# Performance work log

Hardware: AMD Instinct MI355X
Metric: run time of the kernel (lower is better)

## Reference

```python
import jax, jax.numpy as jnp
import numpy as np

T_MEDIA = 3      # torch.arange(3)
N_LATENTS = 64   # repeat(..., m=64)
H = 8            # rearrange h=8
D_HEAD = 64


def setup_inputs() -> dict:
    key = jax.random.key(0)
    ks = jax.random.split(key, 6)
    B, S = 4, 2048
    Dv, Dt = 2048, 4096
    inner = H * D_HEAD  # 512
    latent = jax.random.normal(ks[0], (B, T_MEDIA, N_LATENTS, Dv), dtype=jnp.float32)
    y = jax.random.normal(ks[1], (B, S, Dt), dtype=jnp.float32)
    media_mask = jax.random.randint(ks[2], (B, S), 0, T_MEDIA + 1)  # values in {0,1,2,3}
    W_vk = jax.random.normal(ks[3], (Dv, 2 * inner), dtype=jnp.float32) / np.sqrt(Dv)
    W_q = jax.random.normal(ks[4], (Dt, inner), dtype=jnp.float32) / np.sqrt(Dt)
    W_out = jax.random.normal(ks[5], (inner, Dt), dtype=jnp.float32) / np.sqrt(inner)
    return {"latent": latent, "y": y, "media_mask": media_mask,
            "W_vk": W_vk, "W_q": W_q, "W_out": W_out}


def reference(latent, y, media_mask, W_vk, W_q, W_out):
    B, T, N, Dv = latent.shape
    S = y.shape[1]
    # b t n d -> b (t n) d
    vf = latent.reshape(B, T * N, Dv)
    kv = vf @ W_vk                      # [B, TN, 2*H*Dh]
    k, v = jnp.split(kv, 2, axis=-1)
    q = y @ W_q                         # [B, S, H*Dh]
    def to_heads(x):
        b, n, _ = x.shape
        return x.reshape(b, n, H, D_HEAD).transpose(0, 2, 1, 3)  # b h n d
    q, k, v = to_heads(q), to_heads(k), to_heads(v)
    # NOTE: original applies no 1/sqrt(d) scaling (self.temp unused)
    sim = jnp.einsum('bhid,bhjd->bhij', q, k)   # [B, H, S, T*N]
    media_time = jnp.arange(T) + 1                               # [T]
    key_time = jnp.repeat(media_time, N)                         # [T*N]
    t2m = media_mask[:, None, :, None] == key_time[None, None, None, :]
    neg = -jnp.finfo(sim.dtype).max
    sim = jnp.where(t2m, sim, neg)
    logits = jax.nn.softmax(sim, axis=-1)
    no_media = (media_mask == 0)[:, None, :, None]
    logits = jnp.where(no_media, 0.0, logits)
    out = jnp.einsum('bhij,bhjd->bhid', logits, v)               # [B, H, S, Dh]
    out = out.transpose(0, 2, 1, 3).reshape(B, S, H * D_HEAD)
    return out @ W_out
```

## Files before the change

kernel.cpp:

```cpp
#include <hip/hip_runtime.h>
#include <hip/hip_bf16.h>

typedef __attribute__((ext_vector_type(4))) float f32x4;
typedef __attribute__((ext_vector_type(8))) short bf16x8;
typedef __attribute__((ext_vector_type(4))) unsigned short u16x4;
typedef __attribute__((ext_vector_type(8))) unsigned short u16x8;

#define QCAP 8256
#define QSTR ((size_t)QCAP * 512)
#define KVB 384

__device__ __forceinline__ unsigned short f2bf(float f) {
  unsigned int u = __builtin_bit_cast(unsigned int, f);
  unsigned int r = (u + 0x7FFFu + ((u >> 16) & 1u)) >> 16;
  return (unsigned short)r;
}
__device__ __forceinline__ float bf2f(unsigned short h) {
  unsigned int u = ((unsigned int)h) << 16;
  return __builtin_bit_cast(float, u);
}

__device__ __forceinline__ void gload_lds16(const void* g, void* l) {
  __builtin_amdgcn_global_load_lds(
      (__attribute__((address_space(1))) unsigned int*)g,
      (__attribute__((address_space(3))) unsigned int*)l, 16, 0, 0);
}

__global__ __launch_bounds__(256) void gather_rows(const int* __restrict__ mask,
                                                   int* __restrict__ cnt,
                                                   int* __restrict__ idx,
                                                   int* __restrict__ mcnt,
                                                   int* __restrict__ mlist) {
  int g = blockIdx.x * 256 + threadIdx.x;
  int m = mask[g];
  if (m > 0) {
    int bt = (g >> 11) * 3 + m - 1;
    int p = atomicAdd(&cnt[bt], 1);
    idx[bt * 2048 + p] = g;
  } else {
    int p = atomicAdd(mcnt, 1);
    mlist[p] = g;
  }
}

__global__ __launch_bounds__(256) void scan_build(const int* __restrict__ cnt,
                                                  int* __restrict__ offs,
                                                  const int* __restrict__ idx,
                                                  int* __restrict__ glob) {
  __shared__ int so[13];
  if (threadIdx.x == 0) {
    int s = 0;
#pragma unroll
    for (int i = 0; i < 12; ++i) {
      so[i] = s;
      s += cnt[i];
    }
    so[12] = s;
    if (blockIdx.x == 0)
#pragma unroll
      for (int i = 0; i < 13; ++i) offs[i] = so[i];
  }
  __syncthreads();
  int bt = blockIdx.x;
  int n = cnt[bt], o = so[bt];
  for (int j = threadIdx.x; j < n; j += 256) glob[o + j] = idx[bt * 2048 + j];
}

__global__ __launch_bounds__(256) void prep_all(
    const float* __restrict__ y, const int* __restrict__ glob,
    const int* __restrict__ offs, unsigned short* __restrict__ ybf,
    const float* __restrict__ Wq, const float* __restrict__ Wvk,
    const float* __restrict__ Wo, const float* __restrict__ latent,
    unsigned short* __restrict__ QTh, unsigned short* __restrict__ VKh,
    unsigned short* __restrict__ VKl, unsigned short* __restrict__ OTh,
    unsigned short* __restrict__ latbf) {
  int bid = blockIdx.x;
  if (bid < 16384) {
    int p = bid >> 1, half = bid & 1;
    if (p >= offs[12]) return;
    int g = glob[p];
    const float* src = y + (size_t)g * 4096 + half * 2048 + threadIdx.x * 8;
    unsigned short* dst = ybf + (size_t)p * 4096 + half * 2048 + threadIdx.x * 8;
    f32x4 a = *(const f32x4*)src;
    f32x4 b = *(const f32x4*)(src + 4);
    u16x8 o;
#pragma unroll
    for (int j = 0; j < 4; ++j) o[j] = f2bf(a[j]);
#pragma unroll
    for (int j = 0; j < 4; ++j) o[4 + j] = f2bf(b[j]);
    *(u16x8*)dst = o;
    return;
  }
  if (bid >= 22528) {
    long i = ((long)(bid - 22528) * 256 + threadIdx.x) * 8;
    f32x4 a = *(const f32x4*)(latent + i);
    f32x4 b = *(const f32x4*)(latent + i + 4);
    u16x8 o;
#pragma unroll
    for (int j = 0; j < 4; ++j) o[j] = f2bf(a[j]);
#pragma unroll
    for (int j = 0; j < 4; ++j) o[4 + j] = f2bf(b[j]);
    *(u16x8*)(latbf + i) = o;
    return;
  }
  int wb = bid - 16384;
  __shared__ float tile[32][33];
  const float* W;
  unsigned short *Th, *Tl;
  int K, N, nbx, b;
  if (wb < 2048) {
    W = Wq; Th = QTh; Tl = nullptr; K = 4096; N = 512; nbx = 16; b = wb;
  } else if (wb < 4096) {
    W = Wvk; Th = VKh; Tl = VKl; K = 2048; N = 1024; nbx = 32; b = wb - 2048;
  } else {
    W = Wo; Th = OTh; Tl = nullptr; K = 512; N = 4096; nbx = 128; b = wb - 4096;
  }
  int n0 = (b % nbx) * 32, k0 = (b / nbx) * 32;
  int tx = threadIdx.x & 31, ty = threadIdx.x >> 5;
#pragma unroll
  for (int r = 0; r < 4; ++r)
    tile[ty + 8 * r][tx] = W[(size_t)(k0 + ty + 8 * r) * N + n0 + tx];
  __syncthreads();
#pragma unroll
  for (int r = 0; r < 4; ++r) {
    float f = tile[tx][ty + 8 * r];
    unsigned short hi = f2bf(f);
    size_t o = (size_t)(n0 + ty + 8 * r) * K + k0 + tx;
    Th[o] = hi;
    if (Tl) Tl[o] = f2bf(f - bf2f(hi));
  }
}

__global__ __launch_bounds__(256) void kv_finish(const float* __restrict__ kvp,
                                                 unsigned short* __restrict__ Kh,
                                                 unsigned short* __restrict__ Kl,
                                                 unsigned short* __restrict__ Vt) {
  int row = blockIdx.x;
  int bt = row >> 6, key = row & 63;
  int c = threadIdx.x * 4;
  const float* p = kvp + (size_t)row * 1024 + c;
  f32x4 v = *(const f32x4*)p;
#pragma unroll
  for (int sl = 1; sl < 8; ++sl)
    v += *(const f32x4*)(p + (size_t)sl * 768 * 1024);
  if (c < 512) {
    int h = c >> 6, d = c & 63;
    u16x4 hv, lv;
#pragma unroll
    for (int j = 0; j < 4; ++j) {
      unsigned short hi = f2bf(v[j]);
      hv[j] = hi;
      lv[j] = f2bf(v[j] - bf2f(hi));
    }
    size_t o = ((size_t)(bt * 8 + h) * 64 + key) * 64 + d;
    *(u16x4*)&Kh[o] = hv;
    *(u16x4*)&Kl[o] = lv;
  } else {
    int cc = c - 512;
    int h = cc >> 6, d = cc & 63;
#pragma unroll
    for (int j = 0; j < 4; ++j)
      Vt[((size_t)(bt * 8 + h) * 64 + d + j) * 64 + key] = f2bf(v[j]);
  }
}

#define BM 128
#define BN 128
#define BK 64

__global__ __launch_bounds__(256) void gemm_dual(
    const unsigned short* __restrict__ latbf, const unsigned short* __restrict__ VKh,
    const unsigned short* __restrict__ VKl, const unsigned short* __restrict__ ybf,
    const unsigned short* __restrict__ QTh, float* __restrict__ kvp,
    float* __restrict__ qc, const int* __restrict__ offs) {
  __shared__ unsigned short smem[BM * BK + BN * BK + 64];
  unsigned short* Ald = smem;
  unsigned short* Bhld = smem + BM * BK;
  float* epi = (float*)smem;

  int tid = threadIdx.x, lane = tid & 63, wid = tid >> 6;
  int wr = wid >> 1, wc = wid & 1;
  const unsigned short *Ab, *Bb;
  float* Cv;
  int N, K, kbeg, kend, bm, bn;
  size_t outOff;
  if (blockIdx.x < KVB) {
    int w = (blockIdx.x & 7) * (KVB >> 3) + (blockIdx.x >> 3);
    bm = w / 64;
    int r = w % 64;
    bn = r >> 3;
    int slice = r & 7, ks = slice & 3;
    Ab = latbf + (size_t)(bm * BM) * 2048;
    Bb = (slice < 4 ? VKh : VKl) + (size_t)(bn * BN) * 2048;
    Cv = kvp;
    N = 1024;
    K = 2048;
    kbeg = ks * 512;
    kend = kbeg + 512;
    outOff = (size_t)slice * 768 * 1024;
  } else {
    int qb = blockIdx.x - KVB;
    int w = (qb & 7) * 64 + (qb >> 3);
    bm = w & 63;
    int r = w >> 6;
    bn = r >> 1;
    int ks = r & 1;
    if (bm * BM >= offs[12]) return;
    Ab = ybf + (size_t)(bm * BM) * 4096;
    Bb = QTh + (size_t)(bn * BN) * 4096;
    Cv = qc;
    N = 512;
    K = 4096;
    kbeg = ks * 2048;
    kend = kbeg + 2048;
    outOff = (size_t)ks * QSTR;
  }

  int fr = lane & 15, fq = lane >> 4;
  int srow = lane >> 3, scol = ((lane & 7) ^ (lane >> 3)) * 8;

  f32x4 acc[4][4];
#pragma unroll
  for (int i = 0; i < 4; ++i)
#pragma unroll
    for (int j = 0; j < 4; ++j) acc[i][j] = (f32x4){0.f, 0.f, 0.f, 0.f};

  for (int k0 = kbeg; k0 < kend; k0 += BK) {
#pragma unroll
    for (int i = 0; i < 4; ++i) {
      int c = wid * 4 + i;
      size_t go = (size_t)(c * 8 + srow) * K + k0 + scol;
      gload_lds16(Ab + go, &Ald[c * 512]);
      gload_lds16(Bb + go, &Bhld[c * 512]);
    }
    __syncthreads();
#pragma unroll
    for (int kk = 0; kk < 2; ++kk) {
      int ca = (kk * 32 + fq * 8) ^ ((fr & 7) * 8);
      bf16x8 af[4], bf[4];
#pragma unroll
      for (int i = 0; i < 4; ++i) {
        af[i] = *(const bf16x8*)&Ald[(wr * 64 + i * 16 + fr) * BK + ca];
        bf[i] = *(const bf16x8*)&Bhld[(wc * 64 + i * 16 + fr) * BK + ca];
      }
#pragma unroll
      for (int mi = 0; mi < 4; ++mi)
#pragma unroll
        for (int ni = 0; ni < 4; ++ni)
          acc[mi][ni] = __builtin_amdgcn_mfma_f32_16x16x32_bf16(
              af[mi], bf[ni], acc[mi][ni], 0, 0, 0);
    }
    __syncthreads();
  }

#pragma unroll 1
  for (int p = 0; p < 2; ++p) {
    __syncthreads();
    if (wr == p) {
#pragma unroll
      for (int mi = 0; mi < 4; ++mi)
#pragma unroll
        for (int ni = 0; ni < 4; ++ni)
#pragma unroll
          for (int r = 0; r < 4; ++r) {
            int lrow = mi * 16 + fq * 4 + r;
            int lcol = wc * 64 + ni * 16 + fr;
            int pc = lcol ^ ((lrow & 7) << 4);
            epi[lrow * 128 + pc] = acc[mi][ni][r];
          }
    }
    __syncthreads();
#pragma unroll
    for (int k = 0; k < 8; ++k) {
      int chunk = k * 256 + tid;
      int lrow = chunk >> 5;
      int c4 = (chunk & 31) * 4;
      int pc4 = c4 ^ ((lrow & 7) << 4);
      f32x4 v = *(f32x4*)&epi[lrow * 128 + pc4];
      int row = bm * BM + p * 64 + lrow;
      *(f32x4*)&Cv[outOff + (size_t)row * N + bn * BN + c4] = v;
    }
  }
}

__global__ __launch_bounds__(256) void gemm_out(
    const unsigned short* __restrict__ A, const unsigned short* __restrict__ Bh,
    float* __restrict__ Cv, const int* __restrict__ glob,
    const int* __restrict__ offs, const int* __restrict__ mcnt,
    const int* __restrict__ mlist, int M, int N, int K) {
  __shared__ unsigned short smem[BM * BK + BN * BK + 64];
  unsigned short* Ald = smem;
  unsigned short* Bhld = smem + BM * BK;
  float* epi = (float*)smem;

  int tid = threadIdx.x, lane = tid & 63, wid = tid >> 6;
  int wr = wid >> 1, wc = wid & 1;
  int nwg = gridDim.x;
  int w = (blockIdx.x & 7) * (nwg >> 3) + (blockIdx.x >> 3);
  int nTN = N / BN;
  int nBM = M / BM;
  int bm = w % nBM;
  int bn = w / nBM;
  int mv = offs[12];

  if (bm * BM >= mv) {
    int bmLive = (mv + BM - 1) / BM;
    int nDead = (nBM - bmLive) * nTN;
    int deadIdx = (bm - bmLive) + bn * (nBM - bmLive);
    int nm = *mcnt;
    f32x4 z = (f32x4){0.f, 0.f, 0.f, 0.f};
    for (int j = deadIdx; j < nm; j += nDead) {
      float* row = Cv + (size_t)mlist[j] * N;
#pragma unroll
      for (int i = 0; i < 4; ++i) *(f32x4*)&row[(i * 256 + tid) * 4] = z;
    }
    return;
  }

  const unsigned short* Ab = A + (size_t)(bm * BM) * K;
  const unsigned short* Bhb = Bh + (size_t)(bn * BN) * K;
  int fr = lane & 15, fq = lane >> 4;
  int srow = lane >> 3, scol = ((lane & 7) ^ (lane >> 3)) * 8;

  f32x4 acc[4][4];
#pragma unroll
  for (int i = 0; i < 4; ++i)
#pragma unroll
    for (int j = 0; j < 4; ++j) acc[i][j] = (f32x4){0.f, 0.f, 0.f, 0.f};

  for (int k0 = 0; k0 < K; k0 += BK) {
#pragma unroll
    for (int i = 0; i < 4; ++i) {
      int c = wid * 4 + i;
      size_t go = (size_t)(c * 8 + srow) * K + k0 + scol;
      gload_lds16(Ab + go, &Ald[c * 512]);
      gload_lds16(Bhb + go, &Bhld[c * 512]);
    }
    __syncthreads();
#pragma unroll
    for (int kk = 0; kk < 2; ++kk) {
      int ca = (kk * 32 + fq * 8) ^ ((fr & 7) * 8);
      bf16x8 af[4], bf[4];
#pragma unroll
      for (int i = 0; i < 4; ++i) {
        af[i] = *(const bf16x8*)&Ald[(wr * 64 + i * 16 + fr) * BK + ca];
        bf[i] = *(const bf16x8*)&Bhld[(wc * 64 + i * 16 + fr) * BK + ca];
      }
#pragma unroll
      for (int mi = 0; mi < 4; ++mi)
#pragma unroll
        for (int ni = 0; ni < 4; ++ni)
          acc[mi][ni] = __builtin_amdgcn_mfma_f32_16x16x32_bf16(
              af[mi], bf[ni], acc[mi][ni], 0, 0, 0);
    }
    __syncthreads();
  }

#pragma unroll 1
  for (int p = 0; p < 2; ++p) {
    __syncthreads();
    if (wr == p) {
#pragma unroll
      for (int mi = 0; mi < 4; ++mi)
#pragma unroll
        for (int ni = 0; ni < 4; ++ni)
#pragma unroll
          for (int r = 0; r < 4; ++r) {
            int lrow = mi * 16 + fq * 4 + r;
            int lcol = wc * 64 + ni * 16 + fr;
            int pc = lcol ^ ((lrow & 7) << 4);
            epi[lrow * 128 + pc] = acc[mi][ni][r];
          }
    }
    __syncthreads();
#pragma unroll
    for (int k = 0; k < 8; ++k) {
      int chunk = k * 256 + tid;
      int lrow = chunk >> 5;
      int c4 = (chunk & 31) * 4;
      int pc4 = c4 ^ ((lrow & 7) << 4);
      f32x4 v = *(f32x4*)&epi[lrow * 128 + pc4];
      int row = bm * BM + p * 64 + lrow;
      if (row < mv)
        *(f32x4*)&Cv[(size_t)glob[row] * N + bn * BN + c4] = v;
    }
  }

  int bmLive = (mv + BM - 1) / BM;
  if (bmLive == nBM && bm == 0) {
    int nm = *mcnt;
    f32x4 z = (f32x4){0.f, 0.f, 0.f, 0.f};
    for (int j = bn; j < nm; j += nTN) {
      float* row = Cv + (size_t)mlist[j] * N;
#pragma unroll
      for (int i = 0; i < 4; ++i) *(f32x4*)&row[(i * 256 + tid) * 4] = z;
    }
  }
}

__global__ __launch_bounds__(256) void attn5(
    const float* __restrict__ qc, const unsigned short* __restrict__ Kh,
    const unsigned short* __restrict__ Kl, const unsigned short* __restrict__ Vt,
    const int* __restrict__ cnt, const int* __restrict__ offs,
    unsigned short* __restrict__ attnc) {
  __shared__ unsigned short Pl[4][32][72];
  int tid = threadIdx.x, wid = tid >> 6, lane = tid & 63;
  int fr = lane & 15, fq = lane >> 4;
  int bt = blockIdx.x >> 6, rt = blockIdx.x & 63;
  int n = cnt[bt];
  int rbase = rt * 32;
  if (rbase >= n) return;
  int qbase = offs[bt] + rbase;

#pragma unroll 1
  for (int hp = 0; hp < 2; ++hp) {
    int h = wid * 2 + hp;
    const unsigned short* khb = Kh + ((size_t)(bt * 8 + h) * 64) * 64;
    const unsigned short* klb = Kl + ((size_t)(bt * 8 + h) * 64) * 64;
    const unsigned short* vtb = Vt + ((size_t)(bt * 8 + h) * 64) * 64;

    f32x4 sacc[2][4];
#pragma unroll
    for (int i = 0; i < 2; ++i)
#pragma unroll
      for (int j = 0; j < 4; ++j) sacc[i][j] = (f32x4){0.f, 0.f, 0.f, 0.f};

#pragma unroll
    for (int kk = 0; kk < 2; ++kk) {
      bf16x8 qh[2], ql[2];
#pragma unroll
      for (int mi = 0; mi < 2; ++mi) {
        size_t qo = (size_t)(qbase + mi * 16 + fr) * 512 + h * 64 + kk * 32 + fq * 8;
        f32x4 s0 = *(const f32x4*)(qc + qo) + *(const f32x4*)(qc + QSTR + qo);
        f32x4 s1 = *(const f32x4*)(qc + qo + 4) +
                   *(const f32x4*)(qc + QSTR + qo + 4);
        float sv[8];
        *(f32x4*)&sv[0] = s0;
        *(f32x4*)&sv[4] = s1;
#pragma unroll
        for (int j = 0; j < 8; ++j) {
          unsigned short hi = f2bf(sv[j]);
          qh[mi][j] = (short)hi;
          ql[mi][j] = (short)f2bf(sv[j] - bf2f(hi));
        }
      }
#pragma unroll
      for (int ni = 0; ni < 4; ++ni) {
        size_t ko = (size_t)(ni * 16 + fr) * 64 + kk * 32 + fq * 8;
        bf16x8 kh = *(const bf16x8*)(khb + ko);
        bf16x8 kl = *(const bf16x8*)(klb + ko);
#pragma unroll
        for (int mi = 0; mi < 2; ++mi) {
          sacc[mi][ni] = __builtin_amdgcn_mfma_f32_16x16x32_bf16(
              qh[mi], kh, sacc[mi][ni], 0, 0, 0);
          sacc[mi][ni] = __builtin_amdgcn_mfma_f32_16x16x32_bf16(
              qh[mi], kl, sacc[mi][ni], 0, 0, 0);
          sacc[mi][ni] = __builtin_amdgcn_mfma_f32_16x16x32_bf16(
              ql[mi], kh, sacc[mi][ni], 0, 0, 0);
        }
      }
    }

#pragma unroll
    for (int mi = 0; mi < 2; ++mi) {
#pragma unroll
      for (int r = 0; r < 4; ++r) {
        float m = fmaxf(fmaxf(sacc[mi][0][r], sacc[mi][1][r]),
                        fmaxf(sacc[mi][2][r], sacc[mi][3][r]));
#pragma unroll
        for (int o = 1; o < 16; o <<= 1) m = fmaxf(m, __shfl_xor(m, o));
        float e0 = __expf(sacc[mi][0][r] - m);
        float e1 = __expf(sacc[mi][1][r] - m);
        float e2 = __expf(sacc[mi][2][r] - m);
        float e3 = __expf(sacc[mi][3][r] - m);
        float s = e0 + e1 + e2 + e3;
#pragma unroll
        for (int o = 1; o < 16; o <<= 1) s += __shfl_xor(s, o);
        float inv = 1.f / s;
        int row = mi * 16 + fq * 4 + r;
        Pl[wid][row][fr] = f2bf(e0 * inv);
        Pl[wid][row][16 + fr] = f2bf(e1 * inv);
        Pl[wid][row][32 + fr] = f2bf(e2 * inv);
        Pl[wid][row][48 + fr] = f2bf(e3 * inv);
      }
    }

    f32x4 oacc[2][4];
#pragma unroll
    for (int i = 0; i < 2; ++i)
#pragma unroll
      for (int j = 0; j < 4; ++j) oacc[i][j] = (f32x4){0.f, 0.f, 0.f, 0.f};
#pragma unroll
    for (int kk = 0; kk < 2; ++kk) {
      bf16x8 pa[2];
#pragma unroll
      for (int mi = 0; mi < 2; ++mi)
        pa[mi] = *(const bf16x8*)&Pl[wid][mi * 16 + fr][kk * 32 + fq * 8];
#pragma unroll
      for (int ni = 0; ni < 4; ++ni) {
        bf16x8 vb = *(const bf16x8*)(vtb + (size_t)(ni * 16 + fr) * 64 +
                                     kk * 32 + fq * 8);
#pragma unroll
        for (int mi = 0; mi < 2; ++mi)
          oacc[mi][ni] = __builtin_amdgcn_mfma_f32_16x16x32_bf16(
              pa[mi], vb, oacc[mi][ni], 0, 0, 0);
      }
    }

#pragma unroll
    for (int mi = 0; mi < 2; ++mi)
#pragma unroll
      for (int r = 0; r < 4; ++r) {
        int row = mi * 16 + fq * 4 + r;
        if (rbase + row < n) {
          unsigned short* ar = attnc + (size_t)(qbase + row) * 512 + h * 64 + fr;
          ar[0] = f2bf(oacc[mi][0][r]);
          ar[16] = f2bf(oacc[mi][1][r]);
          ar[32] = f2bf(oacc[mi][2][r]);
          ar[48] = f2bf(oacc[mi][3][r]);
        }
      }
  }
}

extern "C" void kernel_launch(void* const* d_in, const int* in_sizes, int n_in,
                              void* d_out, int out_size, void* d_ws,
                              size_t ws_size, hipStream_t stream) {
  const float* latent = (const float*)d_in[0];
  const float* y = (const float*)d_in[1];
  const int* mask = (const int*)d_in[2];
  const float* W_vk = (const float*)d_in[3];
  const float* W_q = (const float*)d_in[4];
  const float* W_out = (const float*)d_in[5];
  float* out = (float*)d_out;

  char* ws = (char*)d_ws;
  size_t off = 0;
  auto alloc = [&](size_t bytes) -> void* {
    void* p = ws + off;
    off = (off + bytes + 255) & ~(size_t)255;
    return p;
  };
  unsigned short* WqT_h = (unsigned short*)alloc((size_t)512 * 4096 * 2);
  unsigned short* WvkT_h = (unsigned short*)alloc((size_t)1024 * 2048 * 2);
  unsigned short* WvkT_l = (unsigned short*)alloc((size_t)1024 * 2048 * 2);
  unsigned short* WoT_h = (unsigned short*)alloc((size_t)4096 * 512 * 2);
  unsigned short* ybf = (unsigned short*)alloc((size_t)8192 * 4096 * 2);
  unsigned short* latbf = (unsigned short*)alloc((size_t)768 * 2048 * 2);
  float* qc = (float*)alloc((size_t)2 * QCAP * 512 * 4);
  float* kvp = (float*)alloc((size_t)8 * 768 * 1024 * 4);
  unsigned short* Khb = (unsigned short*)alloc((size_t)768 * 512 * 2);
  unsigned short* Klb = (unsigned short*)alloc((size_t)768 * 512 * 2);
  unsigned short* Vtb = (unsigned short*)alloc((size_t)768 * 512 * 2);
  unsigned short* attnc = (unsigned short*)alloc((size_t)8192 * 512 * 2);
  int* cntm = (int*)alloc(13 * 4);
  int* cnt = cntm;
  int* mcnt = cntm + 12;
  int* idx = (int*)alloc((size_t)12 * 2048 * 4);
  int* offs = (int*)alloc(13 * 4);
  int* glob = (int*)alloc(8192 * 4);
  int* mlist = (int*)alloc(8192 * 4);

  hipMemsetAsync(cntm, 0, 13 * 4, stream);

  gather_rows<<<32, 256, 0, stream>>>(mask, cnt, idx, mcnt, mlist);
  scan_build<<<12, 256, 0, stream>>>(cnt, offs, idx, glob);

  prep_all<<<23296, 256, 0, stream>>>(y, glob, offs, ybf, W_q, W_vk, W_out,
                                      latent, WqT_h, WvkT_h, WvkT_l, WoT_h,
                                      latbf);

  gemm_dual<<<KVB + 512, 256, 0, stream>>>(latbf, WvkT_h, WvkT_l, ybf, WqT_h,
                                           kvp, qc, offs);
  kv_finish<<<768, 256, 0, stream>>>(kvp, Khb, Klb, Vtb);
  attn5<<<12 * 64, 256, 0, stream>>>(qc, Khb, Klb, Vtb, cnt, offs, attnc);
  gemm_out<<<(8192 / BM) * (4096 / BN), 256, 0, stream>>>(
      attnc, WoT_h, out, glob, offs, mcnt, mlist, 8192, 4096, 512);
}
```

Baseline: 264.8 us.

## Fuse KV split-K reduction into GEMM epilogue and merge gather/scan kernels

The KV projection no longer splits K into 8 slices written to a float partial buffer and reduced by a separate kv_finish kernel. Each of 48 blocks now accumulates the full K over both hi and lo weight passes and writes the bf16 K hi/lo and transposed V directly from registers. The gather and scan kernels plus the memset are replaced by one single-block kernel that uses shared-memory counters. This drops two launches and the partial-sum traffic, but KV parallelism falls from 384 to 48 blocks with a longer serial K loop, and the epilogue uses scattered 2-byte stores.

Result: faster. 211.8 us (median of 2 runs) (-20.0%).

```diff
diff --git a/kernel.cpp b/kernel.cpp
--- a/kernel.cpp
+++ b/kernel.cpp
@@ -3,12 +3,11 @@
 
 typedef __attribute__((ext_vector_type(4))) float f32x4;
 typedef __attribute__((ext_vector_type(8))) short bf16x8;
-typedef __attribute__((ext_vector_type(4))) unsigned short u16x4;
 typedef __attribute__((ext_vector_type(8))) unsigned short u16x8;
 
 #define QCAP 8256
 #define QSTR ((size_t)QCAP * 512)
-#define KVB 384
+#define KVB 48
 
 __device__ __forceinline__ unsigned short f2bf(float f) {
   unsigned int u = __builtin_bit_cast(unsigned int, f);
@@ -26,44 +25,49 @@
       (__attribute__((address_space(3))) unsigned int*)l, 16, 0, 0);
 }
 
-__global__ __launch_bounds__(256) void gather_rows(const int* __restrict__ mask,
-                                                   int* __restrict__ cnt,
-                                                   int* __restrict__ idx,
-                                                   int* __restrict__ mcnt,
-                                                   int* __restrict__ mlist) {
-  int g = blockIdx.x * 256 + threadIdx.x;
-  int m = mask[g];
-  if (m > 0) {
-    int bt = (g >> 11) * 3 + m - 1;
-    int p = atomicAdd(&cnt[bt], 1);
-    idx[bt * 2048 + p] = g;
-  } else {
-    int p = atomicAdd(mcnt, 1);
-    mlist[p] = g;
-  }
-}
-
-__global__ __launch_bounds__(256) void scan_build(const int* __restrict__ cnt,
-                                                  int* __restrict__ offs,
-                                                  const int* __restrict__ idx,
-                                                  int* __restrict__ glob) {
+__global__ __launch_bounds__(1024) void gather_scan(
+    const int* __restrict__ mask, int* __restrict__ offs,
+    int* __restrict__ glob, int* __restrict__ mcnt, int* __restrict__ mlist) {
+  __shared__ int scnt[13];
   __shared__ int so[13];
-  if (threadIdx.x == 0) {
+  int tid = threadIdx.x;
+  if (tid < 13) scnt[tid] = 0;
+  __syncthreads();
+#pragma unroll
+  for (int i = 0; i < 8; ++i) {
+    int g = i * 1024 + tid;
+    int m = mask[g];
+    atomicAdd(&scnt[m > 0 ? (g >> 11) * 3 + m - 1 : 12], 1);
+  }
+  __syncthreads();
+  if (tid == 0) {
     int s = 0;
 #pragma unroll
     for (int i = 0; i < 12; ++i) {
       so[i] = s;
-      s += cnt[i];
+      s += scnt[i];
     }
     so[12] = s;
-    if (blockIdx.x == 0)
-#pragma unroll
-      for (int i = 0; i < 13; ++i) offs[i] = so[i];
+#pragma unroll
+    for (int i = 0; i < 13; ++i) offs[i] = so[i];
+    *mcnt = scnt[12];
   }
   __syncthreads();
-  int bt = blockIdx.x;
-  int n = cnt[bt], o = so[bt];
-  for (int j = threadIdx.x; j < n; j += 256) glob[o + j] = idx[bt * 2048 + j];
+  if (tid < 13) scnt[tid] = 0;
+  __syncthreads();
+#pragma unroll
+  for (int i = 0; i < 8; ++i) {
+    int g = i * 1024 + tid;
+    int m = mask[g];
+    if (m > 0) {
+      int bt = (g >> 11) * 3 + m - 1;
+      int p = atomicAdd(&scnt[bt], 1);
+      glob[so[bt] + p] = g;
+    } else {
+      int p = atomicAdd(&scnt[12], 1);
+      mlist[p] = g;
+    }
+  }
 }
 
 __global__ __launch_bounds__(256) void prep_all(
@@ -131,39 +135,6 @@
   }
 }
 
-__global__ __launch_bounds__(256) void kv_finish(const float* __restrict__ kvp,
-                                                 unsigned short* __restrict__ Kh,
-                                                 unsigned short* __restrict__ Kl,
-                                                 unsigned short* __restrict__ Vt) {
-  int row = blockIdx.x;
-  int bt = row >> 6, key = row & 63;
-  int c = threadIdx.x * 4;
-  const float* p = kvp + (size_t)row * 1024 + c;
-  f32x4 v = *(const f32x4*)p;
-#pragma unroll
-  for (int sl = 1; sl < 8; ++sl)
-    v += *(const f32x4*)(p + (size_t)sl * 768 * 1024);
-  if (c < 512) {
-    int h = c >> 6, d = c & 63;
-    u16x4 hv, lv;
-#pragma unroll
-    for (int j = 0; j < 4; ++j) {
-      unsigned short hi = f2bf(v[j]);
-      hv[j] = hi;
-      lv[j] = f2bf(v[j] - bf2f(hi));
-    }
-    size_t o = ((size_t)(bt * 8 + h) * 64 + key) * 64 + d;
-    *(u16x4*)&Kh[o] = hv;
-    *(u16x4*)&Kl[o] = lv;
-  } else {
-    int cc = c - 512;
-    int h = cc >> 6, d = cc & 63;
-#pragma unroll
-    for (int j = 0; j < 4; ++j)
-      Vt[((size_t)(bt * 8 + h) * 64 + d + j) * 64 + key] = f2bf(v[j]);
-  }
-}
-
 #define BM 128
 #define BN 128
 #define BK 64
@@ -171,7 +142,8 @@
 __global__ __launch_bounds__(256) void gemm_dual(
     const unsigned short* __restrict__ latbf, const unsigned short* __restrict__ VKh,
     const unsigned short* __restrict__ VKl, const unsigned short* __restrict__ ybf,
-    const unsigned short* __restrict__ QTh, float* __restrict__ kvp,
+    const unsigned short* __restrict__ QTh, unsigned short* __restrict__ Kh,
+    unsigned short* __restrict__ Kl, unsigned short* __restrict__ Vt,
     float* __restrict__ qc, const int* __restrict__ offs) {
   __shared__ unsigned short smem[BM * BK + BN * BK + 64];
   unsigned short* Ald = smem;
@@ -180,40 +152,31 @@
 
   int tid = threadIdx.x, lane = tid & 63, wid = tid >> 6;
   int wr = wid >> 1, wc = wid & 1;
-  const unsigned short *Ab, *Bb;
-  float* Cv;
-  int N, K, kbeg, kend, bm, bn;
-  size_t outOff;
-  if (blockIdx.x < KVB) {
-    int w = (blockIdx.x & 7) * (KVB >> 3) + (blockIdx.x >> 3);
-    bm = w / 64;
-    int r = w % 64;
-    bn = r >> 3;
-    int slice = r & 7, ks = slice & 3;
+  bool isKV = blockIdx.x < KVB;
+  const unsigned short* Ab;
+  const unsigned short* Bb = nullptr;
+  int K, kbeg, kend, bm, bn, ks = 0;
+  if (isKV) {
+    int sw = (blockIdx.x & 7) * (KVB >> 3) + (blockIdx.x >> 3);
+    bm = sw / 8;
+    bn = sw % 8;
     Ab = latbf + (size_t)(bm * BM) * 2048;
-    Bb = (slice < 4 ? VKh : VKl) + (size_t)(bn * BN) * 2048;
-    Cv = kvp;
-    N = 1024;
     K = 2048;
-    kbeg = ks * 512;
-    kend = kbeg + 512;
-    outOff = (size_t)slice * 768 * 1024;
+    kbeg = 0;
+    kend = 2048;
   } else {
     int qb = blockIdx.x - KVB;
     int w = (qb & 7) * 64 + (qb >> 3);
     bm = w & 63;
     int r = w >> 6;
     bn = r >> 1;
-    int ks = r & 1;
+    ks = r & 1;
     if (bm * BM >= offs[12]) return;
     Ab = ybf + (size_t)(bm * BM) * 4096;
     Bb = QTh + (size_t)(bn * BN) * 4096;
-    Cv = qc;
-    N = 512;
     K = 4096;
     kbeg = ks * 2048;
     kend = kbeg + 2048;
-    outOff = (size_t)ks * QSTR;
   }
 
   int fr = lane & 15, fq = lane >> 4;
@@ -225,32 +188,64 @@
 #pragma unroll
     for (int j = 0; j < 4; ++j) acc[i][j] = (f32x4){0.f, 0.f, 0.f, 0.f};
 
-  for (int k0 = kbeg; k0 < kend; k0 += BK) {
-#pragma unroll
-    for (int i = 0; i < 4; ++i) {
-      int c = wid * 4 + i;
-      size_t go = (size_t)(c * 8 + srow) * K + k0 + scol;
-      gload_lds16(Ab + go, &Ald[c * 512]);
-      gload_lds16(Bb + go, &Bhld[c * 512]);
-    }
-    __syncthreads();
-#pragma unroll
-    for (int kk = 0; kk < 2; ++kk) {
-      int ca = (kk * 32 + fq * 8) ^ ((fr & 7) * 8);
-      bf16x8 af[4], bf[4];
+  int npass = isKV ? 2 : 1;
+#pragma unroll 1
+  for (int pass = 0; pass < npass; ++pass) {
+    const unsigned short* Bp =
+        isKV ? ((pass ? VKl : VKh) + (size_t)(bn * BN) * 2048) : Bb;
+    for (int k0 = kbeg; k0 < kend; k0 += BK) {
 #pragma unroll
       for (int i = 0; i < 4; ++i) {
-        af[i] = *(const bf16x8*)&Ald[(wr * 64 + i * 16 + fr) * BK + ca];
-        bf[i] = *(const bf16x8*)&Bhld[(wc * 64 + i * 16 + fr) * BK + ca];
-      }
-#pragma unroll
-      for (int mi = 0; mi < 4; ++mi)
-#pragma unroll
-        for (int ni = 0; ni < 4; ++ni)
-          acc[mi][ni] = __builtin_amdgcn_mfma_f32_16x16x32_bf16(
-              af[mi], bf[ni], acc[mi][ni], 0, 0, 0);
-    }
-    __syncthreads();
+        int c = wid * 4 + i;
+        size_t go = (size_t)(c * 8 + srow) * K + k0 + scol;
+        gload_lds16(Ab + go, &Ald[c * 512]);
+        gload_lds16(Bp + go, &Bhld[c * 512]);
+      }
+      __syncthreads();
+#pragma unroll
+      for (int kk = 0; kk < 2; ++kk) {
+        int ca = (kk * 32 + fq * 8) ^ ((fr & 7) * 8);
+        bf16x8 af[4], bf[4];
+#pragma unroll
+        for (int i = 0; i < 4; ++i) {
+          af[i] = *(const bf16x8*)&Ald[(wr * 64 + i * 16 + fr) * BK + ca];
+          bf[i] = *(const bf16x8*)&Bhld[(wc * 64 + i * 16 + fr) * BK + ca];
+        }
+#pragma unroll
+        for (int mi = 0; mi < 4; ++mi)
+#pragma unroll
+          for (int ni = 0; ni < 4; ++ni)
+            acc[mi][ni] = __builtin_amdgcn_mfma_f32_16x16x32_bf16(
+                af[mi], bf[ni], acc[mi][ni], 0, 0, 0);
+      }
+      __syncthreads();
+    }
+  }
+
+  if (isKV) {
+#pragma unroll
+    for (int mi = 0; mi < 4; ++mi)
+#pragma unroll
+      for (int ni = 0; ni < 4; ++ni)
+#pragma unroll
+        for (int r = 0; r < 4; ++r) {
+          int row = bm * BM + wr * 64 + mi * 16 + fq * 4 + r;
+          int col = bn * BN + wc * 64 + ni * 16 + fr;
+          int bt = row >> 6, key = row & 63;
+          float v = acc[mi][ni][r];
+          if (col < 512) {
+            int h = col >> 6, d = col & 63;
+            unsigned short hi = f2bf(v);
+            size_t o = ((size_t)(bt * 8 + h) * 64 + key) * 64 + d;
+            Kh[o] = hi;
+            Kl[o] = f2bf(v - bf2f(hi));
+          } else {
+            int c = col - 512;
+            int h = c >> 6, d = c & 63;
+            Vt[((size_t)(bt * 8 + h) * 64 + d) * 64 + key] = f2bf(v);
+          }
+        }
+    return;
   }
 
 #pragma unroll 1
@@ -278,7 +273,7 @@
       int pc4 = c4 ^ ((lrow & 7) << 4);
       f32x4 v = *(f32x4*)&epi[lrow * 128 + pc4];
       int row = bm * BM + p * 64 + lrow;
-      *(f32x4*)&Cv[outOff + (size_t)row * N + bn * BN + c4] = v;
+      *(f32x4*)&qc[(size_t)ks * QSTR + (size_t)row * 512 + bn * BN + c4] = v;
     }
   }
 }
@@ -401,13 +396,12 @@
 __global__ __launch_bounds__(256) void attn5(
     const float* __restrict__ qc, const unsigned short* __restrict__ Kh,
     const unsigned short* __restrict__ Kl, const unsigned short* __restrict__ Vt,
-    const int* __restrict__ cnt, const int* __restrict__ offs,
-    unsigned short* __restrict__ attnc) {
+    const int* __restrict__ offs, unsigned short* __restrict__ attnc) {
   __shared__ unsigned short Pl[4][32][72];
   int tid = threadIdx.x, wid = tid >> 6, lane = tid & 63;
   int fr = lane & 15, fq = lane >> 4;
   int bt = blockIdx.x >> 6, rt = blockIdx.x & 63;
-  int n = cnt[bt];
+  int n = offs[bt + 1] - offs[bt];
   int rbase = rt * 32;
   if (rbase >= n) return;
   int qbase = offs[bt] + rbase;
@@ -548,32 +542,24 @@
   unsigned short* ybf = (unsigned short*)alloc((size_t)8192 * 4096 * 2);
   unsigned short* latbf = (unsigned short*)alloc((size_t)768 * 2048 * 2);
   float* qc = (float*)alloc((size_t)2 * QCAP * 512 * 4);
-  float* kvp = (float*)alloc((size_t)8 * 768 * 1024 * 4);
   unsigned short* Khb = (unsigned short*)alloc((size_t)768 * 512 * 2);
   unsigned short* Klb = (unsigned short*)alloc((size_t)768 * 512 * 2);
   unsigned short* Vtb = (unsigned short*)alloc((size_t)768 * 512 * 2);
   unsigned short* attnc = (unsigned short*)alloc((size_t)8192 * 512 * 2);
-  int* cntm = (int*)alloc(13 * 4);
-  int* cnt = cntm;
-  int* mcnt = cntm + 12;
-  int* idx = (int*)alloc((size_t)12 * 2048 * 4);
   int* offs = (int*)alloc(13 * 4);
   int* glob = (int*)alloc(8192 * 4);
+  int* mcnt = (int*)alloc(4);
   int* mlist = (int*)alloc(8192 * 4);
 
-  hipMemsetAsync(cntm, 0, 13 * 4, stream);
-
-  gather_rows<<<32, 256, 0, stream>>>(mask, cnt, idx, mcnt, mlist);
-  scan_build<<<12, 256, 0, stream>>>(cnt, offs, idx, glob);
+  gather_scan<<<1, 1024, 0, stream>>>(mask, offs, glob, mcnt, mlist);
 
   prep_all<<<23296, 256, 0, stream>>>(y, glob, offs, ybf, W_q, W_vk, W_out,
                                       latent, WqT_h, WvkT_h, WvkT_l, WoT_h,
                                       latbf);
 
   gemm_dual<<<KVB + 512, 256, 0, stream>>>(latbf, WvkT_h, WvkT_l, ybf, WqT_h,
-                                           kvp, qc, offs);
-  kv_finish<<<768, 256, 0, stream>>>(kvp, Khb, Klb, Vtb);
-  attn5<<<12 * 64, 256, 0, stream>>>(qc, Khb, Klb, Vtb, cnt, offs, attnc);
+                                           Khb, Klb, Vtb, qc, offs);
+  attn5<<<12 * 64, 256, 0, stream>>>(qc, Khb, Klb, Vtb, offs, attnc);
   gemm_out<<<(8192 / BM) * (4096 / BN), 256, 0, stream>>>(
       attnc, WoT_h, out, glob, offs, mcnt, mlist, 8192, 4096, 512);
 }
```
